# Optimization experiments

Measured on AMD Instinct MI355X. Metric: run time of the kernel, lower is better.

Reference implementation:

```python
import jax, jax.numpy as jnp
import numpy as np

VOCAB, EMB, HID, OUT = 10, 32, 64, 10
B, T = 4096, 128

def setup_inputs() -> dict:
    key = jax.random.key(0)
    ks = jax.random.split(key, 8)
    num1 = jax.random.randint(ks[0], (B, T), 0, VOCAB, dtype=jnp.int32)
    num2 = jax.random.randint(ks[1], (B, T), 0, VOCAB, dtype=jnp.int32)
    # Glorot-ish scaled params (values irrelevant for correctness baseline)
    E = jax.random.normal(ks[2], (VOCAB, EMB), jnp.float32) * 0.05
    Wxh = jax.random.normal(ks[3], (2 * EMB, HID), jnp.float32) * (1.0 / np.sqrt(2 * EMB))
    Whh = jax.random.normal(ks[4], (HID, HID), jnp.float32) * (1.0 / np.sqrt(HID))
    b = jax.random.normal(ks[5], (HID,), jnp.float32) * 0.01
    Wd = jax.random.normal(ks[6], (HID, OUT), jnp.float32) * (1.0 / np.sqrt(HID))
    bd = jax.random.normal(ks[7], (OUT,), jnp.float32) * 0.01
    return {"num1": num1, "num2": num2, "E": E, "Wxh": Wxh, "Whh": Whh,
            "b": b, "Wd": Wd, "bd": bd}

def reference(num1, num2, E, Wxh, Whh, b, Wd, bd):
    # Embedding lookup + concat: [B, T, 2*EMB]
    x = jnp.concatenate([E[num1], E[num2]], axis=-1)
    # Precompute input projection for all timesteps (batched GEMM)
    xp = jnp.einsum('bti,ih->bth', x, Wxh) + b  # [B, T, HID]
    h0 = jnp.zeros((x.shape[0], Whh.shape[0]), x.dtype)

    def step(h, xt):  # SimpleRNNCell: h' = tanh(x W_xh + b + h W_hh)
        h = jnp.tanh(xt + h @ Whh)
        return h, h

    _, hs = jax.lax.scan(step, h0, jnp.swapaxes(xp, 0, 1))  # [T, B, HID]
    rnn_out = jnp.swapaxes(hs, 0, 1)  # return_sequences=True -> [B, T, HID]
    logits = rnn_out @ Wd + bd  # [B, T, 10]
    return logits
```

## Files before the change

kernel.cpp:

```cpp
#include <hip/hip_runtime.h>


typedef _Float16 half8 __attribute__((ext_vector_type(8)));
typedef __fp16 fp16x2 __attribute__((ext_vector_type(2)));
typedef float floatx4 __attribute__((ext_vector_type(4)));

#define MFMA16(A, B, C) __builtin_amdgcn_mfma_f32_16x16x32_f16((A), (B), (C), 0, 0, 0)
#define BARRIER() asm volatile("s_waitcnt lgkmcnt(0)\n\ts_barrier" ::: "memory")

#define LUT_DW  17408
#define PKM_DW  18432
#define POOL_DW 20544
#define NPS_DW  6528

__global__ __launch_bounds__(512)
void rnn_mfma(const int* __restrict__ num1, const int* __restrict__ num2,
              const float* __restrict__ E, const float* __restrict__ Wxh,
              const float* __restrict__ Whh, const float* __restrict__ bias,
              const float* __restrict__ Wd, const float* __restrict__ bd,
              float* __restrict__ out)
{
    __shared__ __align__(16) int pool[POOL_DW];
    int* lutI  = pool + LUT_DW;
    int* pkm   = pool + PKM_DW;
    int* npS   = pool + NPS_DW;

    const int tid  = threadIdx.x;
    const int wv   = tid >> 6;
    const bool prod = (wv < 4);
    const int w    = wv & 3;
    const int lane = tid & 63;
    const int c    = lane & 15;
    const int q    = lane >> 4;
    const int qs   = q * 8;
    const int g    = blockIdx.x;

    float* WhhS = (float*)pool;
    float* P1t  = (float*)(pool + 4096);
    float* P2t  = (float*)(pool + 4736);
    float* WdS  = (float*)(pool + 5376);
    for (int i = tid; i < 4096; i += 512) WhhS[i] = Whh[i];
    for (int i = tid; i < 640;  i += 512) WdS[i]  = Wd[i];
    for (int idx = tid; idx < 640; idx += 512) {
        int v = idx >> 6, jj = idx & 63;
        float s1 = bias[jj], s2 = 0.f;
        #pragma unroll
        for (int i = 0; i < 32; ++i) {
            float e = E[v * 32 + i];
            s1 = fmaf(e, Wxh[i * 64 + jj], s1);
            s2 = fmaf(e, Wxh[(32 + i) * 64 + jj], s2);
        }
        P1t[idx] = s1;
        P2t[idx] = s2;
    }
    if (tid < 256) {
        int e = tid;
        #pragma unroll
        for (int j = 0; j < 4; ++j)
            lutI[e * 4 + j] = (((e >> (2 * j)) & 1) ? 0x3C00 : 0)
                            | (((e >> (2 * j + 1)) & 1) ? 0x3C000000 : 0);
    }
    for (int idx = tid; idx < 2048; idx += 512) {
        int m = idx & 15, t = idx >> 4;
        int s = g * 16 + m;
        npS[t * 16 + m] = (1 << num1[s * 128 + t]) | (1 << (num2[s * 128 + t] + 10));
    }
    __syncthreads();

    for (int idx = tid; idx < 64 * 33; idx += 512) {
        int l  = idx & 63;
        int tt = idx >> 6;
        int lc = l & 15, lqs = (l >> 4) * 8;
        unsigned dw = 0;
        #pragma unroll
        for (int k = 0; k < 4; ++k) {
            int t = tt * 4 + k;
            unsigned byte = (t < 128) ? ((unsigned)(npS[t * 16 + lc] >> lqs) & 0xFFu) : 0u;
            dw |= byte << (8 * k);
        }
        pkm[l * 33 + tt] = (int)dw;
    }

    half8 Wint[4], Wdint[4], Pf;
    float bdv = 0.f;
    if (prod) {
        #pragma unroll
        for (int kt = 0; kt < 4; ++kt)
            #pragma unroll
            for (int p = 0; p < 4; ++p) {
                int k = kt * 16 + q * 4 + p;
                float wvv = WhhS[k * 64 + w * 16 + c];
                Wint[kt][2 * p]     = (_Float16)wvv;
                Wint[kt][2 * p + 1] = (_Float16)(wvv * 0.015625f);
            }
        #pragma unroll
        for (int j = 0; j < 8; ++j) {
            int i2 = qs + j;
            float pv = (i2 < 10) ? P1t[i2 * 64 + w * 16 + c]
                     : (i2 < 20) ? P2t[(i2 - 10) * 64 + w * 16 + c] : 0.f;
            Pf[j] = (_Float16)pv;
        }
    } else {
        #pragma unroll
        for (int kt = 0; kt < 4; ++kt)
            #pragma unroll
            for (int p = 0; p < 4; ++p) {
                int k = kt * 16 + q * 4 + p;
                float dv = (c < 10) ? WdS[k * 10 + c] : 0.f;
                Wdint[kt][2 * p]     = (_Float16)dv;
                Wdint[kt][2 * p + 1] = (_Float16)(dv * 0.015625f);
            }
        bdv = (c < 10) ? bd[c] : 0.f;
    }
    __syncthreads();

    for (int i = tid; i < 1088; i += 512) pool[15 * 1088 + i] = 0;
    __syncthreads();

    const int rBase = c * 68 + q * 4;
    const floatx4 zero4 = {0.f, 0.f, 0.f, 0.f};

    if (prod) {
        const int wBase  = (q * 4) * 68 + w * 16 + c;
        const int pkBase = lane * 33;

        floatx4 Cxp;
        {
            unsigned b0 = (unsigned)pkm[pkBase] & 0xFFu;
            half8 Aoh = *(const half8*)&lutI[b0 * 4];
            Cxp = MFMA16(Aoh, Pf, zero4);
        }

        for (int half = 0; half < 16; ++half) {
            const int sb = (half & 1) * 8;
            int d0 = pkm[pkBase + 2 * half];
            int d1 = pkm[pkBase + 2 * half + 1];
            int d2 = pkm[pkBase + 2 * half + 2];
            #pragma unroll
            for (int i = 0; i < 8; ++i) {
                const int spw = sb + i;
                const int spr = (i == 0) ? ((sb ^ 8) + 7) : (sb + i - 1);

                half8 A0 = *(const half8*)&pool[spr * 1088 + rBase];
                half8 A1 = *(const half8*)&pool[spr * 1088 + rBase + 16];
                half8 A2 = *(const half8*)&pool[spr * 1088 + rBase + 32];
                half8 A3 = *(const half8*)&pool[spr * 1088 + rBase + 48];
                unsigned b = (i < 3) ? (((unsigned)d0 >> (8 * (i + 1))) & 0xFFu)
                           : (i < 7) ? (((unsigned)d1 >> (8 * (i - 3))) & 0xFFu)
                                     : ((unsigned)d2 & 0xFFu);
                half8 Aoh = *(const half8*)&lutI[b * 4];

                floatx4 Ca = MFMA16(A0, Wint[0], Cxp);
                floatx4 Cb = MFMA16(A1, Wint[1], zero4);
                floatx4 Cc = MFMA16(A2, Wint[2], zero4);
                floatx4 Cd = MFMA16(A3, Wint[3], zero4);
                Cxp = MFMA16(Aoh, Pf, zero4);

                float hv[4];
                #pragma unroll
                for (int r = 0; r < 4; ++r) {
                    float x  = (Ca[r] + Cb[r]) + (Cc[r] + Cd[r]);
                    float e2 = __builtin_amdgcn_exp2f(x * 2.885390081777927f);
                    hv[r] = 1.f - 2.f * __builtin_amdgcn_rcpf(e2 + 1.f);
                }
                #pragma unroll
                for (int p = 0; p < 2; ++p) {
                    fp16x2 ph = __builtin_amdgcn_cvt_pkrtz(hv[2 * p], hv[2 * p + 1]);
                    float c0 = (float)ph[0];
                    float c1 = (float)ph[1];
                    fp16x2 pl = __builtin_amdgcn_cvt_pkrtz((hv[2 * p] - c0) * 64.f,
                                                           (hv[2 * p + 1] - c1) * 64.f);
                    unsigned phu = __builtin_bit_cast(unsigned, ph);
                    unsigned plu = __builtin_bit_cast(unsigned, pl);
                    unsigned w0 = __builtin_amdgcn_perm(plu, phu, 0x05040100u);
                    unsigned w1 = __builtin_amdgcn_perm(plu, phu, 0x07060302u);
                    pool[spw * 1088 + wBase + (2 * p) * 68]     = (int)w0;
                    pool[spw * 1088 + wBase + (2 * p + 1) * 68] = (int)w1;
                }

                BARRIER();
            }
        }
    } else {
        float* outP[2][4];
        #pragma unroll
        for (int u = 0; u < 2; ++u)
            #pragma unroll
            for (int r = 0; r < 4; ++r)
                outP[u][r] = out + (((g * 16 + q * 4 + r) * 128) + 2 * w + u) * 10 + c;
        const bool cLt10 = (c < 10);

        for (int ph = 0; ph < 16; ++ph) {
            const int sbp = (ph & 1) ? 0 : 8;
            #pragma unroll
            for (int i = 0; i < 8; ++i) {
                if (ph > 0 && (i == w || i == w + 4)) {
                    const int u  = (i == w) ? 0 : 1;
                    const int sl = (sbp + 2 * w + u) * 1088 + rBase;
                    half8 P0 = *(const half8*)&pool[sl];
                    half8 P1 = *(const half8*)&pool[sl + 16];
                    half8 P2 = *(const half8*)&pool[sl + 32];
                    half8 P3 = *(const half8*)&pool[sl + 48];
                    floatx4 Cp = MFMA16(P0, Wdint[0], zero4);
                    Cp         = MFMA16(P1, Wdint[1], Cp);
                    Cp         = MFMA16(P2, Wdint[2], Cp);
                    Cp         = MFMA16(P3, Wdint[3], Cp);
                    if (cLt10) {
                        #pragma unroll
                        for (int r = 0; r < 4; ++r)
                            outP[u][r][0] = Cp[r] + bdv;
                    }
                }
                BARRIER();
            }
            if (ph > 0) {
                #pragma unroll
                for (int u = 0; u < 2; ++u)
                    #pragma unroll
                    for (int r = 0; r < 4; ++r)
                        outP[u][r] += 80;
            }
        }

        #pragma unroll
        for (int u = 0; u < 2; ++u) {
            const int sl = (8 + 2 * w + u) * 1088 + rBase;
            half8 P0 = *(const half8*)&pool[sl];
            half8 P1 = *(const half8*)&pool[sl + 16];
            half8 P2 = *(const half8*)&pool[sl + 32];
            half8 P3 = *(const half8*)&pool[sl + 48];
            floatx4 Cp = MFMA16(P0, Wdint[0], zero4);
            Cp         = MFMA16(P1, Wdint[1], Cp);
            Cp         = MFMA16(P2, Wdint[2], Cp);
            Cp         = MFMA16(P3, Wdint[3], Cp);
            if (cLt10) {
                #pragma unroll
                for (int r = 0; r < 4; ++r)
                    outP[u][r][0] = Cp[r] + bdv;
            }
        }
    }
}

extern "C" void kernel_launch(void* const* d_in, const int* in_sizes, int n_in,
                              void* d_out, int out_size, void* d_ws, size_t ws_size,
                              hipStream_t stream) {
    const int*   num1 = (const int*)d_in[0];
    const int*   num2 = (const int*)d_in[1];
    const float* E    = (const float*)d_in[2];
    const float* Wxh  = (const float*)d_in[3];
    const float* Whh  = (const float*)d_in[4];
    const float* b    = (const float*)d_in[5];
    const float* Wd   = (const float*)d_in[6];
    const float* bd   = (const float*)d_in[7];
    float* out = (float*)d_out;
    rnn_mfma<<<256, 512, 0, stream>>>(num1, num2, E, Wxh, Whh, b, Wd, bd, out);
}
```

Baseline: 112.8 us.

## Drop split-fp16 hidden state, use plain fp16 for recurrence and output

Replaces the hi/lo split-fp16 encoding of the hidden state, which doubled the K dimension so compensated MFMAs could keep near-fp32 accuracy, with plain fp16 storage. This halves the recurrent and output MFMAs per step, halves the LDS reads and shared-memory footprint, and removes the pack/perm conversion code. The cost is lower precision in the 128-step recurrence, since fp16 rounding error can accumulate through Whh and may exceed tolerance.

```diff
diff --git a/kernel.cpp b/kernel.cpp
--- a/kernel.cpp
+++ b/kernel.cpp
@@ -2,15 +2,14 @@
 
 
 typedef _Float16 half8 __attribute__((ext_vector_type(8)));
-typedef __fp16 fp16x2 __attribute__((ext_vector_type(2)));
 typedef float floatx4 __attribute__((ext_vector_type(4)));
 
 #define MFMA16(A, B, C) __builtin_amdgcn_mfma_f32_16x16x32_f16((A), (B), (C), 0, 0, 0)
 #define BARRIER() asm volatile("s_waitcnt lgkmcnt(0)\n\ts_barrier" ::: "memory")
 
-#define LUT_DW  17408
-#define PKM_DW  18432
-#define POOL_DW 20544
+#define LUT_DW  8704
+#define PKM_DW  9728
+#define POOL_DW 11840
 #define NPS_DW  6528
 
 __global__ __launch_bounds__(512)
@@ -21,9 +20,10 @@
               float* __restrict__ out)
 {
     __shared__ __align__(16) int pool[POOL_DW];
-    int* lutI  = pool + LUT_DW;
-    int* pkm   = pool + PKM_DW;
-    int* npS   = pool + NPS_DW;
+    _Float16* hiF = (_Float16*)pool;
+    int* lutI = pool + LUT_DW;
+    int* pkm  = pool + PKM_DW;
+    int* npS  = pool + NPS_DW;
 
     const int tid  = threadIdx.x;
     const int wv   = tid >> 6;
@@ -81,18 +81,14 @@
         pkm[l * 33 + tt] = (int)dw;
     }
 
-    half8 Wint[4], Wdint[4], Pf;
+    half8 Wf[2], Wdf[2], Pf;
     float bdv = 0.f;
     if (prod) {
         #pragma unroll
-        for (int kt = 0; kt < 4; ++kt)
-            #pragma unroll
-            for (int p = 0; p < 4; ++p) {
-                int k = kt * 16 + q * 4 + p;
-                float wvv = WhhS[k * 64 + w * 16 + c];
-                Wint[kt][2 * p]     = (_Float16)wvv;
-                Wint[kt][2 * p + 1] = (_Float16)(wvv * 0.015625f);
-            }
+        for (int kt = 0; kt < 2; ++kt)
+            #pragma unroll
+            for (int j = 0; j < 8; ++j)
+                Wf[kt][j] = (_Float16)WhhS[(kt * 32 + qs + j) * 64 + w * 16 + c];
         #pragma unroll
         for (int j = 0; j < 8; ++j) {
             int i2 = qs + j;
@@ -102,26 +98,23 @@
         }
     } else {
         #pragma unroll
-        for (int kt = 0; kt < 4; ++kt)
-            #pragma unroll
-            for (int p = 0; p < 4; ++p) {
-                int k = kt * 16 + q * 4 + p;
-                float dv = (c < 10) ? WdS[k * 10 + c] : 0.f;
-                Wdint[kt][2 * p]     = (_Float16)dv;
-                Wdint[kt][2 * p + 1] = (_Float16)(dv * 0.015625f);
-            }
+        for (int kt = 0; kt < 2; ++kt)
+            #pragma unroll
+            for (int j = 0; j < 8; ++j)
+                Wdf[kt][j] = (c < 10) ? (_Float16)WdS[(kt * 32 + qs + j) * 10 + c]
+                                      : (_Float16)0.f;
         bdv = (c < 10) ? bd[c] : 0.f;
     }
     __syncthreads();
 
-    for (int i = tid; i < 1088; i += 512) pool[15 * 1088 + i] = 0;
+    for (int i = tid; i < 544; i += 512) pool[15 * 544 + i] = 0;
     __syncthreads();
 
-    const int rBase = c * 68 + q * 4;
+    const int rvE = c * 68 + qs;
     const floatx4 zero4 = {0.f, 0.f, 0.f, 0.f};
 
     if (prod) {
-        const int wBase  = (q * 4) * 68 + w * 16 + c;
+        const int wvE    = (q * 4) * 68 + w * 16 + c;
         const int pkBase = lane * 33;
 
         floatx4 Cxp;
@@ -141,41 +134,23 @@
                 const int spw = sb + i;
                 const int spr = (i == 0) ? ((sb ^ 8) + 7) : (sb + i - 1);
 
-                half8 A0 = *(const half8*)&pool[spr * 1088 + rBase];
-                half8 A1 = *(const half8*)&pool[spr * 1088 + rBase + 16];
-                half8 A2 = *(const half8*)&pool[spr * 1088 + rBase + 32];
-                half8 A3 = *(const half8*)&pool[spr * 1088 + rBase + 48];
+                half8 A0 = *(const half8*)&hiF[spr * 1088 + rvE];
+                half8 A1 = *(const half8*)&hiF[spr * 1088 + rvE + 32];
                 unsigned b = (i < 3) ? (((unsigned)d0 >> (8 * (i + 1))) & 0xFFu)
                            : (i < 7) ? (((unsigned)d1 >> (8 * (i - 3))) & 0xFFu)
                                      : ((unsigned)d2 & 0xFFu);
                 half8 Aoh = *(const half8*)&lutI[b * 4];
 
-                floatx4 Ca = MFMA16(A0, Wint[0], Cxp);
-                floatx4 Cb = MFMA16(A1, Wint[1], zero4);
-                floatx4 Cc = MFMA16(A2, Wint[2], zero4);
-                floatx4 Cd = MFMA16(A3, Wint[3], zero4);
+                floatx4 Ca = MFMA16(A0, Wf[0], Cxp);
+                floatx4 Cb = MFMA16(A1, Wf[1], zero4);
                 Cxp = MFMA16(Aoh, Pf, zero4);
 
-                float hv[4];
                 #pragma unroll
                 for (int r = 0; r < 4; ++r) {
-                    float x  = (Ca[r] + Cb[r]) + (Cc[r] + Cd[r]);
+                    float x  = Ca[r] + Cb[r];
                     float e2 = __builtin_amdgcn_exp2f(x * 2.885390081777927f);
-                    hv[r] = 1.f - 2.f * __builtin_amdgcn_rcpf(e2 + 1.f);
-                }
-                #pragma unroll
-                for (int p = 0; p < 2; ++p) {
-                    fp16x2 ph = __builtin_amdgcn_cvt_pkrtz(hv[2 * p], hv[2 * p + 1]);
-                    float c0 = (float)ph[0];
-                    float c1 = (float)ph[1];
-                    fp16x2 pl = __builtin_amdgcn_cvt_pkrtz((hv[2 * p] - c0) * 64.f,
-                                                           (hv[2 * p + 1] - c1) * 64.f);
-                    unsigned phu = __builtin_bit_cast(unsigned, ph);
-                    unsigned plu = __builtin_bit_cast(unsigned, pl);
-                    unsigned w0 = __builtin_amdgcn_perm(plu, phu, 0x05040100u);
-                    unsigned w1 = __builtin_amdgcn_perm(plu, phu, 0x07060302u);
-                    pool[spw * 1088 + wBase + (2 * p) * 68]     = (int)w0;
-                    pool[spw * 1088 + wBase + (2 * p + 1) * 68] = (int)w1;
+                    float hv = 1.f - 2.f * __builtin_amdgcn_rcpf(e2 + 1.f);
+                    hiF[spw * 1088 + wvE + r * 68] = (_Float16)hv;
                 }
 
                 BARRIER();
@@ -196,15 +171,11 @@
             for (int i = 0; i < 8; ++i) {
                 if (ph > 0 && (i == w || i == w + 4)) {
                     const int u  = (i == w) ? 0 : 1;
-                    const int sl = (sbp + 2 * w + u) * 1088 + rBase;
-                    half8 P0 = *(const half8*)&pool[sl];
-                    half8 P1 = *(const half8*)&pool[sl + 16];
-                    half8 P2 = *(const half8*)&pool[sl + 32];
-                    half8 P3 = *(const half8*)&pool[sl + 48];
-                    floatx4 Cp = MFMA16(P0, Wdint[0], zero4);
-                    Cp         = MFMA16(P1, Wdint[1], Cp);
-                    Cp         = MFMA16(P2, Wdint[2], Cp);
-                    Cp         = MFMA16(P3, Wdint[3], Cp);
+                    const int sl = (sbp + 2 * w + u) * 1088 + rvE;
+                    half8 P0 = *(const half8*)&hiF[sl];
+                    half8 P1 = *(const half8*)&hiF[sl + 32];
+                    floatx4 Cp = MFMA16(P0, Wdf[0], zero4);
+                    Cp         = MFMA16(P1, Wdf[1], Cp);
                     if (cLt10) {
                         #pragma unroll
                         for (int r = 0; r < 4; ++r)
@@ -224,15 +195,11 @@
 
         #pragma unroll
         for (int u = 0; u < 2; ++u) {
-            const int sl = (8 + 2 * w + u) * 1088 + rBase;
-            half8 P0 = *(const half8*)&pool[sl];
-            half8 P1 = *(const half8*)&pool[sl + 16];
-            half8 P2 = *(const half8*)&pool[sl + 32];
-            half8 P3 = *(const half8*)&pool[sl + 48];
-            floatx4 Cp = MFMA16(P0, Wdint[0], zero4);
-            Cp         = MFMA16(P1, Wdint[1], Cp);
-            Cp         = MFMA16(P2, Wdint[2], Cp);
-            Cp         = MFMA16(P3, Wdint[3], Cp);
+            const int sl = (8 + 2 * w + u) * 1088 + rvE;
+            half8 P0 = *(const half8*)&hiF[sl];
+            half8 P1 = *(const half8*)&hiF[sl + 32];
+            floatx4 Cp = MFMA16(P0, Wdf[0], zero4);
+            Cp         = MFMA16(P1, Wdf[1], Cp);
             if (cLt10) {
                 #pragma unroll
                 for (int r = 0; r < 4; ++r)
```

After: 137.5 us. +21.9%, slower.
